# Kernel tuning notes

Measured on AMD Instinct MI355X. Metric: run time of the kernel, lower is better.

Reference implementation:

```python
import jax, jax.numpy as jnp
import numpy as np

K = 0.5   # k constant from init
QS = 0.1  # qs constant from init


def setup_inputs() -> dict:
    key = jax.random.key(0)
    k1, k2, k3 = jax.random.split(key, 3)
    B, OUT, M, IN = 512, 128, 8, 512
    x = jax.random.normal(k1, (B, IN), dtype=jnp.float32)
    W = jax.random.uniform(k2, (OUT, M, IN), dtype=jnp.float32)
    q = jax.random.uniform(k3, (OUT, M, IN), dtype=jnp.float32)
    return {"x": x, "W": W, "q": q}


def reference(x, W, q):
    # x: [B, IN]; W, q: [OUT, M, IN]
    # dendritic: relu(k * (x*W - q)), summed over input dim
    syn = jax.nn.relu(K * (x[:, None, None, :] * W - q))  # [B, OUT, M, IN]
    dend = jax.nn.relu(jnp.sum(syn, axis=3))              # [B, OUT, M]
    soma = jnp.sum(dend, axis=2)                          # [B, OUT]
    return jax.nn.relu(K * (soma - QS))
```

## Files before the change

kernel.cpp:

```cpp
#include <hip/hip_runtime.h>


#define OUTN 128
#define MM   8
#define INN  512

typedef float f4 __attribute__((ext_vector_type(4)));

__global__ __launch_bounds__(256) void dnm_kernel(
    const float* __restrict__ x,
    const float* __restrict__ W,
    const float* __restrict__ q,
    float* __restrict__ out)
{
    __shared__ float lds_w[MM * INN];
    __shared__ float lds_q[MM * INN];

    const int tid  = threadIdx.x;
    const int o    = blockIdx.x >> 4;
    const int bgrp = blockIdx.x & 15;
    const int wave = tid >> 6;
    const int lane = tid & 63;
    const int b0   = bgrp * 32 + wave * 8;

    {
        const f4* Wg = (const f4*)(W + (size_t)o * MM * INN);
        const f4* qg = (const f4*)(q + (size_t)o * MM * INN);
        f4* lw = (f4*)lds_w;
        f4* lq = (f4*)lds_q;
        #pragma unroll
        for (int j = 0; j < (MM * INN / 4); j += 256) {
            lw[j + tid] = Wg[j + tid];
            lq[j + tid] = qg[j + tid];
        }
    }
    __syncthreads();

    f4 acc[8];
    #pragma unroll
    for (int b = 0; b < 8; ++b) acc[b] = (f4)0.0f;

    #pragma unroll 1
    for (int chunk = 0; chunk < 2; ++chunk) {
        const int i = chunk * 256 + lane * 4;

        f4 xv[8];
        #pragma unroll
        for (int b = 0; b < 8; ++b)
            xv[b] = *(const f4*)(x + (size_t)(b0 + b) * INN + i);

        #pragma unroll
        for (int m = 0; m < MM; ++m) {
            const f4 w4 = *(const f4*)(lds_w + m * INN + i);
            const f4 q4 = *(const f4*)(lds_q + m * INN + i);
            #pragma unroll
            for (int b = 0; b < 8; ++b) {
                f4 t = __builtin_elementwise_fma(xv[b], w4, -q4);
                t = __builtin_elementwise_max(t, (f4)0.0f);
                acc[b] += t;
            }
        }
    }

    #pragma unroll
    for (int b = 0; b < 8; ++b) {
        float v = (acc[b].x + acc[b].y) + (acc[b].z + acc[b].w);
        v += __shfl_xor(v, 1, 64);
        v += __shfl_xor(v, 2, 64);
        v += __shfl_xor(v, 4, 64);
        v += __shfl_xor(v, 8, 64);
        v += __shfl_xor(v, 16, 64);
        v += __shfl_xor(v, 32, 64);
        if (lane == b) {
            float r = 0.25f * v - 0.05f;
            out[(size_t)(b0 + b) * OUTN + o] = fmaxf(r, 0.0f);
        }
    }
}

extern "C" void kernel_launch(void* const* d_in, const int* in_sizes, int n_in,
                              void* d_out, int out_size, void* d_ws, size_t ws_size,
                              hipStream_t stream) {
    const float* x = (const float*)d_in[0];
    const float* W = (const float*)d_in[1];
    const float* q = (const float*)d_in[2];
    float* out = (float*)d_out;
    dim3 grid(OUTN * 16);
    dim3 block(256);
    dnm_kernel<<<grid, block, 0, stream>>>(x, W, q, out);
}
```

Before: 81.45 us.

## Convert inputs to fp16 and compute dendritic sums with packed half math

Adds a pre-pass kernel that converts x, W and q to fp16 in the workspace. The main kernel then runs packed half2 FMA and max, and accumulates through fdot2 into fp32. This halves LDS footprint and global traffic and doubles ALU throughput per instruction. The cost is an extra kernel launch and reduced precision in the per-synapse terms, since the relu sums over 512 elements could accumulate noticeable error.

```diff
diff --git a/kernel.cpp b/kernel.cpp
--- a/kernel.cpp
+++ b/kernel.cpp
@@ -5,16 +5,35 @@
 #define MM   8
 #define INN  512
 
-typedef float f4 __attribute__((ext_vector_type(4)));
+typedef float    f4 __attribute__((ext_vector_type(4)));
+typedef float    f2 __attribute__((ext_vector_type(2)));
+typedef _Float16 h2 __attribute__((ext_vector_type(2)));
+typedef _Float16 h4 __attribute__((ext_vector_type(4)));
+typedef _Float16 h8 __attribute__((ext_vector_type(8)));
+
+#define XH_ELEMS 262144
+#define WH_ELEMS 524288
+
+__global__ __launch_bounds__(256) void cvt_kernel(
+    const float* __restrict__ x, const float* __restrict__ W,
+    const float* __restrict__ q, _Float16* __restrict__ h)
+{
+    const int j = blockIdx.x * 256 + threadIdx.x;
+    f4 v;
+    if (j < 65536)        v = ((const f4*)x)[j];
+    else if (j < 196608)  v = ((const f4*)W)[j - 65536];
+    else                  v = ((const f4*)q)[j - 196608];
+    ((h4*)h)[j] = __builtin_convertvector(v, h4);
+}
 
 __global__ __launch_bounds__(256) void dnm_kernel(
-    const float* __restrict__ x,
-    const float* __restrict__ W,
-    const float* __restrict__ q,
+    const _Float16* __restrict__ xh,
+    const _Float16* __restrict__ Wh,
+    const _Float16* __restrict__ qh,
     float* __restrict__ out)
 {
-    __shared__ float lds_w[MM * INN];
-    __shared__ float lds_q[MM * INN];
+    __shared__ _Float16 lds_w[MM * INN];
+    __shared__ _Float16 lds_q[MM * INN];
 
     const int tid  = threadIdx.x;
     const int o    = blockIdx.x >> 4;
@@ -22,49 +41,57 @@
     const int wave = tid >> 6;
     const int lane = tid & 63;
     const int b0   = bgrp * 32 + wave * 8;
+    const int i0   = lane * 8;
 
     {
-        const f4* Wg = (const f4*)(W + (size_t)o * MM * INN);
-        const f4* qg = (const f4*)(q + (size_t)o * MM * INN);
+        const f4* Wg = (const f4*)(Wh + (size_t)o * MM * INN);
+        const f4* qg = (const f4*)(qh + (size_t)o * MM * INN);
         f4* lw = (f4*)lds_w;
         f4* lq = (f4*)lds_q;
-        #pragma unroll
-        for (int j = 0; j < (MM * INN / 4); j += 256) {
-            lw[j + tid] = Wg[j + tid];
-            lq[j + tid] = qg[j + tid];
-        }
+        lw[tid]       = Wg[tid];
+        lw[tid + 256] = Wg[tid + 256];
+        lq[tid]       = qg[tid];
+        lq[tid + 256] = qg[tid + 256];
     }
+
+    h8 xv[8];
+    #pragma unroll
+    for (int b = 0; b < 8; ++b)
+        xv[b] = *(const h8*)(xh + (size_t)(b0 + b) * INN + i0);
+
     __syncthreads();
 
-    f4 acc[8];
+    float acc[8];
     #pragma unroll
-    for (int b = 0; b < 8; ++b) acc[b] = (f4)0.0f;
+    for (int b = 0; b < 8; ++b) acc[b] = 0.0f;
 
-    #pragma unroll 1
-    for (int chunk = 0; chunk < 2; ++chunk) {
-        const int i = chunk * 256 + lane * 4;
+    const h2 one = {(_Float16)1.0f, (_Float16)1.0f};
 
-        f4 xv[8];
+    #pragma unroll 2
+    for (int m = 0; m < MM; ++m) {
+        const h8 w8 = *(const h8*)(lds_w + m * INN + i0);
+        const h8 q8 = *(const h8*)(lds_q + m * INN + i0);
         #pragma unroll
-        for (int b = 0; b < 8; ++b)
-            xv[b] = *(const f4*)(x + (size_t)(b0 + b) * INN + i);
-
-        #pragma unroll
-        for (int m = 0; m < MM; ++m) {
-            const f4 w4 = *(const f4*)(lds_w + m * INN + i);
-            const f4 q4 = *(const f4*)(lds_q + m * INN + i);
+        for (int b = 0; b < 8; ++b) {
             #pragma unroll
-            for (int b = 0; b < 8; ++b) {
-                f4 t = __builtin_elementwise_fma(xv[b], w4, -q4);
-                t = __builtin_elementwise_max(t, (f4)0.0f);
-                acc[b] += t;
+            for (int p = 0; p < 4; ++p) {
+                h2 xx = {xv[b][2 * p], xv[b][2 * p + 1]};
+                h2 ww = {w8[2 * p], w8[2 * p + 1]};
+                h2 qq = {q8[2 * p], q8[2 * p + 1]};
+                h2 t = __builtin_elementwise_fma(xx, ww, -qq);
+                t = __builtin_elementwise_max(t, (h2)(_Float16)0.0f);
+#if __has_builtin(__builtin_amdgcn_fdot2)
+                acc[b] = __builtin_amdgcn_fdot2(t, one, acc[b], false);
+#else
+                acc[b] += (float)t[0] + (float)t[1];
+#endif
             }
         }
     }
 
     #pragma unroll
     for (int b = 0; b < 8; ++b) {
-        float v = (acc[b].x + acc[b].y) + (acc[b].z + acc[b].w);
+        float v = acc[b];
         v += __shfl_xor(v, 1, 64);
         v += __shfl_xor(v, 2, 64);
         v += __shfl_xor(v, 4, 64);
@@ -85,7 +112,12 @@
     const float* W = (const float*)d_in[1];
     const float* q = (const float*)d_in[2];
     float* out = (float*)d_out;
-    dim3 grid(OUTN * 16);
-    dim3 block(256);
-    dnm_kernel<<<grid, block, 0, stream>>>(x, W, q, out);
+    _Float16* h = (_Float16*)d_ws;
+
+    cvt_kernel<<<dim3(1280), dim3(256), 0, stream>>>(x, W, q, h);
+
+    const _Float16* xh = h;
+    const _Float16* Wh = h + XH_ELEMS;
+    const _Float16* qh = h + XH_ELEMS + WH_ELEMS;
+    dnm_kernel<<<dim3(OUTN * 16), dim3(256), 0, stream>>>(xh, Wh, qh, out);
 }
```

Measured after the change: 79.22 us. 1.03x faster.
